# Kernel tuning notes

Measured on AMD Instinct MI355X. Metric: run time of the kernel, lower is better.

The kernel has to match this reference:

```python
import jax, jax.numpy as jnp
import numpy as np

NUM_LAYERS = 2
HIDDEN = 512
INPUT = 512


def _lstm_cell(x, h, c, Wih, Whh, bih, bbh):
    # PyTorch LSTMCell: gates ordered i, f, g, o
    g = x @ Wih.T + bih + h @ Whh.T + bbh  # [B, 4H]
    i, f, gg, o = jnp.split(g, 4, axis=-1)
    c_new = jax.nn.sigmoid(f) * c + jax.nn.sigmoid(i) * jnp.tanh(gg)
    h_new = jax.nn.sigmoid(o) * jnp.tanh(c_new)
    return h_new, c_new


def setup_inputs() -> dict:
    key = jax.random.key(0)
    ks = jax.random.split(key, 8)
    B, T = 64, 512
    s = 1.0 / np.sqrt(HIDDEN)
    return {
        "x": jax.random.normal(ks[0], (B, T, INPUT), dtype=jnp.float32),
        "h0": jax.random.normal(ks[1], (NUM_LAYERS, B, HIDDEN), dtype=jnp.float32),
        "c0": jax.random.normal(ks[2], (NUM_LAYERS, B, HIDDEN), dtype=jnp.float32),
        # stacked per-layer weights (input_size == hidden_size so shapes match)
        "W_ih": jax.random.uniform(ks[3], (NUM_LAYERS, 4 * HIDDEN, INPUT), jnp.float32, -s, s),
        "W_hh": jax.random.uniform(ks[4], (NUM_LAYERS, 4 * HIDDEN, HIDDEN), jnp.float32, -s, s),
        "b_ih": jax.random.uniform(ks[5], (NUM_LAYERS, 4 * HIDDEN), jnp.float32, -s, s),
        "b_hh": jax.random.uniform(ks[6], (NUM_LAYERS, 4 * HIDDEN), jnp.float32, -s, s),
    }


def reference(x, h0, c0, W_ih, W_hh, b_ih, b_hh):
    # x: [B, T, D]; h0/c0: [L, B, H]
    xs = jnp.swapaxes(x, 0, 1)  # [T, B, D] for scan over time

    def step(carry, x_t):
        h, c = carry  # each [L, B, H]
        h_list, c_list = [], []
        inp = x_t
        for j in range(NUM_LAYERS):  # small static unroll over layers
            h_j, c_j = _lstm_cell(inp, h[j], c[j], W_ih[j], W_hh[j], b_ih[j], b_hh[j])
            h_list.append(h_j)
            c_list.append(c_j)
            inp = h_j
        h_new = jnp.stack(h_list, axis=0)
        c_new = jnp.stack(c_list, axis=0)
        return (h_new, c_new), inp  # output of top layer

    (h_fin, c_fin), outs = jax.lax.scan(step, (h0, c0), xs)
    out = jnp.swapaxes(outs, 0, 1)  # [B, T, H]
    return out, h_fin, c_fin
```

## Files before the change

kernel.cpp:

```cpp
#include <hip/hip_runtime.h>
#include <hip/hip_bf16.h>


#define TT 512

using short8 = __attribute__((ext_vector_type(8))) short;
using f32x4  = __attribute__((ext_vector_type(4))) float;

__device__ __forceinline__ short f2bf(float f) {
  unsigned u = __float_as_uint(f);
  u = (u + 0x7fffu + ((u >> 16) & 1u)) >> 16;
  return (short)u;
}
__device__ __forceinline__ float bf2f(short s) {
  return __uint_as_float(((unsigned)(unsigned short)s) << 16);
}
__device__ __forceinline__ float sigf(float x) { return 1.f / (1.f + __expf(-x)); }
__device__ __forceinline__ float tanh_(float x) { return 1.f - 2.f / (__expf(2.f * x) + 1.f); }

__device__ __forceinline__ void ld8_nw(short8* d,
    const short* p0, const short* p1, const short* p2, const short* p3,
    const short* p4, const short* p5, const short* p6, const short* p7) {
  asm volatile(
      "global_load_dwordx4 %0, %8, off sc0 sc1\n\t"
      "global_load_dwordx4 %1, %9, off sc0 sc1\n\t"
      "global_load_dwordx4 %2, %10, off sc0 sc1\n\t"
      "global_load_dwordx4 %3, %11, off sc0 sc1\n\t"
      "global_load_dwordx4 %4, %12, off sc0 sc1\n\t"
      "global_load_dwordx4 %5, %13, off sc0 sc1\n\t"
      "global_load_dwordx4 %6, %14, off sc0 sc1\n\t"
      "global_load_dwordx4 %7, %15, off sc0 sc1"
      : "=&v"(d[0]), "=&v"(d[1]), "=&v"(d[2]), "=&v"(d[3]),
        "=&v"(d[4]), "=&v"(d[5]), "=&v"(d[6]), "=&v"(d[7])
      : "v"(p0), "v"(p1), "v"(p2), "v"(p3),
        "v"(p4), "v"(p5), "v"(p6), "v"(p7)
      : "memory");
}

#define TIE8(A, CNT)                                                        \
  asm volatile(CNT : "+v"(A[0]), "+v"(A[1]), "+v"(A[2]), "+v"(A[3]),        \
                     "+v"(A[4]), "+v"(A[5]), "+v"(A[6]), "+v"(A[7])         \
               ::"memory")

__device__ __forceinline__ void stc_short(short* p, short v) {
  asm volatile("global_store_short %0, %1, off sc0 sc1"
               :: "v"(p), "v"((int)v) : "memory");
}

__global__ __launch_bounds__(256) void conv_x(const float* __restrict__ x,
                                              short* __restrict__ xo) {
  size_t g = (size_t)blockIdx.x * 256 + threadIdx.x;
  size_t i = g * 8;
  float4 v0 = *(const float4*)(x + i);
  float4 v1 = *(const float4*)(x + i + 4);
  short8 r;
  r[0] = f2bf(v0.x); r[1] = f2bf(v0.y); r[2] = f2bf(v0.z); r[3] = f2bf(v0.w);
  r[4] = f2bf(v1.x); r[5] = f2bf(v1.y); r[6] = f2bf(v1.z); r[7] = f2bf(v1.w);
  *(short8*)(xo + (i >> 9) * 1024 + (i & 511)) = r;
}

__global__ __launch_bounds__(256) void conv_w(const float* __restrict__ Wih,
                                              const float* __restrict__ Whh,
                                              short* __restrict__ wp) {
  int g = blockIdx.x * 256 + threadIdx.x;
  int l = g / 393216;
  int rem = g % 393216;
  int j8 = rem / 6144;
  int q8 = rem % 6144;
  int s, hl, bt, c, lane;
  if (q8 < 2048) {
    s = 0; hl = 0;
    int seg = q8 >> 6; bt = seg >> 4; c = seg & 15; lane = q8 & 63;
  } else {
    int q = q8 - 2048;
    s = 1;
    int seg = q >> 6; bt = seg >> 5; c = (seg >> 1) & 15; hl = seg & 1;
    lane = q & 63;
  }
  int r = lane & 15;
  int gg = r >> 2, jj = r & 3;
  int R = gg * 512 + j8 * 8 + bt * 4 + jj;
  int k = c * 32 + (lane >> 4) * 8;
  const float* src = (s ? Whh : Wih) + ((size_t)(l * 2048 + R)) * 512 + k;
  short8 o;
#pragma unroll
  for (int e = 0; e < 8; ++e) {
    float v = src[e];
    short hi = f2bf(v);
    o[e] = hl ? f2bf(v - bf2f(hi)) : hi;
  }
  *(short8*)(wp + (size_t)g * 8) = o;
}

__global__ __launch_bounds__(256) void init_state(const float* __restrict__ h0,
                                                  short* __restrict__ hhi,
                                                  short* __restrict__ hlo,
                                                  unsigned* __restrict__ bar) {
  int i = blockIdx.x * 256 + threadIdx.x;
  int l = i >> 15, bj = i & 32767;
  int b = bj >> 9, j = bj & 511;
  float h = h0[i];
  short hi = f2bf(h);
  int o = (l * 2) * 32768 + (j >> 3) * 512 + b * 8 + (j & 7);
  hhi[o] = hi;
  hlo[o] = f2bf(h - bf2f(hi));
  if (blockIdx.x < 4) bar[blockIdx.x * 256 + threadIdx.x] = 0u;
}

__device__ __forceinline__ void garrive(unsigned* bar, int tid, int slot) {
  __syncthreads();
  if (tid == 0)
    __hip_atomic_fetch_add(&bar[slot * 32], 1u, __ATOMIC_RELAXED,
                           __HIP_MEMORY_SCOPE_AGENT);
}
__device__ __forceinline__ void gwait(unsigned* bar, unsigned target, int tid) {
  if (tid == 0) {
    for (;;) {
      unsigned sum = 0;
#pragma unroll
      for (int r = 0; r < 32; ++r)
        sum += __hip_atomic_load(&bar[r * 32], __ATOMIC_RELAXED,
                                 __HIP_MEMORY_SCOPE_AGENT);
      if (sum >= target) break;
      __builtin_amdgcn_s_sleep(1);
    }
  }
  __syncthreads();
}

__global__ __launch_bounds__(512, 1) void lstm_persist(
    const short* __restrict__ wp, const float* __restrict__ c0,
    const float* __restrict__ bih, const float* __restrict__ bhh,
    short* __restrict__ hhi, short* __restrict__ hlo,
    unsigned* __restrict__ bar, float* __restrict__ out) {
  extern __shared__ char smem[];
  short* lw = (short*)smem;
  float* sG = (float*)(smem + 98304);

  const int tid = threadIdx.x;
  const int layer = blockIdx.x >> 6;
  const int j8 = blockIdx.x & 63;
  const int bslot = blockIdx.x & 31;
  const int wv = tid >> 6;
  const int kq = wv & 3;
  const int ah = wv >> 2;
  const int lane = tid & 63;
  const int m = lane & 15;
  const int koq = lane >> 4;
  const int cbase = kq << 2;

  {
    const short* src = wp + (size_t)(layer * 64 + j8) * 49152;
    for (int i = tid; i < 6144; i += 512)
      *(short8*)(lw + i * 8) = *(const short8*)(src + i * 8);
  }

  const int sb = tid >> 3, sj = tid & 7;
  const int j = (j8 << 3) + sj;
  float creg = c0[layer * 32768 + sb * 512 + j];
  float hf = 0.f;
  float bsum[4];
#pragma unroll
  for (int g = 0; g < 4; ++g)
    bsum[g] = bih[layer * 2048 + g * 512 + j] + bhh[layer * 2048 + g * 512 + j];
  __syncthreads();

  const int br0 = ((ah * 2 + 0) << 4) + m;
  const int br1 = ((ah * 2 + 1) << 4) + m;
  const short* xo = (const short*)out;

  f32x4 acc[2][2];

  auto ih_l0 = [&](int txt) {
#pragma unroll
    for (int cc = 0; cc < 4; ++cc) {
      const int c = cbase + cc;
      const int k = c * 32 + (koq << 3);
      short8 b0 = *(const short8*)(lw + c * 512 + lane * 8);
      short8 b1 = *(const short8*)(lw + (16 + c) * 512 + lane * 8);
#pragma unroll
      for (int it = 0; it < 2; ++it) {
        const int br = it ? br1 : br0;
        short8 a = *(const short8*)(xo + ((size_t)br * TT + txt) * 1024 + k);
        acc[0][it] = __builtin_amdgcn_mfma_f32_16x16x32_bf16(a, b0, acc[0][it], 0, 0, 0);
        acc[1][it] = __builtin_amdgcn_mfma_f32_16x16x32_bf16(a, b1, acc[1][it], 0, 0, 0);
      }
    }
  };

  if (layer == 0) {
#pragma unroll
    for (int u = 0; u < 2; ++u)
#pragma unroll
      for (int v = 0; v < 2; ++v) acc[u][v] = f32x4{0.f, 0.f, 0.f, 0.f};
    ih_l0(0);
  }

#define PA(rX, cc, br) \
  ((rX) + ((((cbase + (cc)) << 2) + koq) << 9) + (br) * 8)

  for (int t = 0; t <= TT; ++t) {
    const int tl = layer ? (t - 1) : t;
    if (tl >= 0 && tl < TT) {
      const int pin = tl & 1, pout = pin ^ 1;
      if (t > 0) gwait(bar, 128u * (unsigned)t, tid);

      short8 Ah[8], Al[8];
      const short* rh = hhi + (layer * 2 + pin) * 32768;
      const short* rl = hlo + (layer * 2 + pin) * 32768;

      if (layer == 0) {
        ld8_nw(Ah, PA(rh, 0, br0), PA(rh, 0, br1), PA(rh, 1, br0), PA(rh, 1, br1),
                   PA(rh, 2, br0), PA(rh, 2, br1), PA(rh, 3, br0), PA(rh, 3, br1));
        ld8_nw(Al, PA(rl, 0, br0), PA(rl, 0, br1), PA(rl, 1, br0), PA(rl, 1, br1),
                   PA(rl, 2, br0), PA(rl, 2, br1), PA(rl, 3, br0), PA(rl, 3, br1));
        TIE8(Ah, "s_waitcnt vmcnt(0)");
        TIE8(Al, "");
      } else {
#pragma unroll
        for (int u = 0; u < 2; ++u)
#pragma unroll
          for (int v = 0; v < 2; ++v) acc[u][v] = f32x4{0.f, 0.f, 0.f, 0.f};
        short8 Ax[8];
        const short* ph = hhi + (t & 1) * 32768;
        ld8_nw(Ax, PA(ph, 0, br0), PA(ph, 0, br1), PA(ph, 1, br0), PA(ph, 1, br1),
                   PA(ph, 2, br0), PA(ph, 2, br1), PA(ph, 3, br0), PA(ph, 3, br1));
        ld8_nw(Ah, PA(rh, 0, br0), PA(rh, 0, br1), PA(rh, 1, br0), PA(rh, 1, br1),
                   PA(rh, 2, br0), PA(rh, 2, br1), PA(rh, 3, br0), PA(rh, 3, br1));
        ld8_nw(Al, PA(rl, 0, br0), PA(rl, 0, br1), PA(rl, 1, br0), PA(rl, 1, br1),
                   PA(rl, 2, br0), PA(rl, 2, br1), PA(rl, 3, br0), PA(rl, 3, br1));
        TIE8(Ax, "s_waitcnt vmcnt(16)");
#pragma unroll
        for (int cc = 0; cc < 4; ++cc) {
          const int c = cbase + cc;
          short8 b0 = *(const short8*)(lw + c * 512 + lane * 8);
          short8 b1 = *(const short8*)(lw + (16 + c) * 512 + lane * 8);
#pragma unroll
          for (int it = 0; it < 2; ++it) {
            short8 a = Ax[cc * 2 + it];
            acc[0][it] = __builtin_amdgcn_mfma_f32_16x16x32_bf16(a, b0, acc[0][it], 0, 0, 0);
            acc[1][it] = __builtin_amdgcn_mfma_f32_16x16x32_bf16(a, b1, acc[1][it], 0, 0, 0);
          }
        }
        TIE8(Ah, "s_waitcnt vmcnt(0)");
        TIE8(Al, "");
      }

#pragma unroll
      for (int cc = 0; cc < 4; ++cc) {
        const int c = cbase + cc;
        short8 bh0 = *(const short8*)(lw + 16384 + (c * 2 + 0) * 512 + lane * 8);
        short8 bl0 = *(const short8*)(lw + 16384 + (c * 2 + 1) * 512 + lane * 8);
        short8 bh1 = *(const short8*)(lw + 16384 + ((16 + c) * 2 + 0) * 512 + lane * 8);
        short8 bl1 = *(const short8*)(lw + 16384 + ((16 + c) * 2 + 1) * 512 + lane * 8);
#pragma unroll
        for (int it = 0; it < 2; ++it) {
          short8 a = Ah[cc * 2 + it];
          short8 al = Al[cc * 2 + it];
          acc[0][it] = __builtin_amdgcn_mfma_f32_16x16x32_bf16(a, bh0, acc[0][it], 0, 0, 0);
          acc[0][it] = __builtin_amdgcn_mfma_f32_16x16x32_bf16(a, bl0, acc[0][it], 0, 0, 0);
          acc[0][it] = __builtin_amdgcn_mfma_f32_16x16x32_bf16(al, bh0, acc[0][it], 0, 0, 0);
          acc[1][it] = __builtin_amdgcn_mfma_f32_16x16x32_bf16(a, bh1, acc[1][it], 0, 0, 0);
          acc[1][it] = __builtin_amdgcn_mfma_f32_16x16x32_bf16(a, bl1, acc[1][it], 0, 0, 0);
          acc[1][it] = __builtin_amdgcn_mfma_f32_16x16x32_bf16(al, bh1, acc[1][it], 0, 0, 0);
        }
      }

#pragma unroll
      for (int bt = 0; bt < 2; ++bt)
#pragma unroll
        for (int it = 0; it < 2; ++it) {
          const int srow = bt * 16 + m;
          const int col = ((ah * 2 + it) << 4) + (koq << 2);
#pragma unroll
          for (int r = 0; r < 4; ++r)
            sG[(kq * 32 + srow) * 66 + col + r] = acc[bt][it][r];
        }
      __syncthreads();

      {
        const int bt = sj >> 2, jl = sj & 3;
        float gv[4];
#pragma unroll
        for (int g = 0; g < 4; ++g) {
          const int s = bt * 16 + g * 4 + jl;
          gv[g] = sG[(0 * 32 + s) * 66 + sb] + sG[(1 * 32 + s) * 66 + sb] +
                  sG[(2 * 32 + s) * 66 + sb] + sG[(3 * 32 + s) * 66 + sb] +
                  bsum[g];
        }
        const float cn = sigf(gv[1]) * creg + sigf(gv[0]) * tanh_(gv[2]);
        const float hn = sigf(gv[3]) * tanh_(cn);
        creg = cn;
        hf = hn;
        const int ho = (layer * 2 + pout) * 32768 + (j8 << 9) + tid;
        const short hb = f2bf(hn);
        stc_short(hhi + ho, hb);
        stc_short(hlo + ho, f2bf(hn - bf2f(hb)));
        if (layer)
          __builtin_nontemporal_store(hn, &out[((size_t)sb * 512 + tl) * 512 + j]);
      }
    }
    if (t < TT) {
      garrive(bar, tid, bslot);
      if (layer == 0 && t + 1 < TT) {
#pragma unroll
        for (int u = 0; u < 2; ++u)
#pragma unroll
          for (int v = 0; v < 2; ++v) acc[u][v] = f32x4{0.f, 0.f, 0.f, 0.f};
        ih_l0(t + 1);
      }
    }
  }

  out[16777216 + layer * 32768 + sb * 512 + j] = hf;
  out[16777216 + 65536 + layer * 32768 + sb * 512 + j] = creg;
}


extern "C" void kernel_launch(void* const* d_in, const int* in_sizes, int n_in,
                              void* d_out, int out_size, void* d_ws,
                              size_t ws_size, hipStream_t stream) {
  const float* x = (const float*)d_in[0];
  const float* h0 = (const float*)d_in[1];
  const float* c0 = (const float*)d_in[2];
  const float* Wih = (const float*)d_in[3];
  const float* Whh = (const float*)d_in[4];
  const float* bih = (const float*)d_in[5];
  const float* bhh = (const float*)d_in[6];
  float* out = (float*)d_out;

  char* ws = (char*)d_ws;
  short* wp = (short*)(ws + 0);
  short* hhi = (short*)(ws + 12582912);
  short* hlo = (short*)(ws + 12845056);
  unsigned* bar = (unsigned*)(ws + 13107200);

  hipFuncSetAttribute(reinterpret_cast<const void*>(lstm_persist),
                      hipFuncAttributeMaxDynamicSharedMemorySize, 132096);

  conv_x<<<8192, 256, 0, stream>>>(x, (short*)out);
  conv_w<<<3072, 256, 0, stream>>>(Wih, Whh, wp);
  init_state<<<256, 256, 0, stream>>>(h0, hhi, hlo, bar);

  void* args[] = {(void*)&wp,  (void*)&c0,  (void*)&bih, (void*)&bhh,
                  (void*)&hhi, (void*)&hlo, (void*)&bar, (void*)&out};
  hipLaunchCooperativeKernel(reinterpret_cast<void*>(lstm_persist), dim3(128),
                             dim3(512), args, 132096, stream);
}
```

Baseline: 2.735 ms.

## Replace global grid barrier with per-block progress flags and layer-decoupled pipelining

Replaces the per-timestep global atomic barrier over all 128 blocks with per-block progress flags that dependent blocks poll. Layer 0 keeps a 4-deep ring of h buffers, so it can run up to three steps ahead of layer 1. Layer 1 waits only on layer 0's step and on its own peers. This is meant to remove global barrier latency and the lockstep coupling between layers. In exchange it adds more polling traffic (64 lanes loading flags) and relies on plain stores plus cache-bypass flags for memory ordering.

```diff
diff --git a/kernel.cpp b/kernel.cpp
--- a/kernel.cpp
+++ b/kernel.cpp
@@ -46,6 +46,29 @@
   asm volatile("global_store_short %0, %1, off sc0 sc1"
                :: "v"(p), "v"((int)v) : "memory");
 }
+__device__ __forceinline__ void stc_int(int* p, int v) {
+  asm volatile("global_store_dword %0, %1, off sc0 sc1"
+               :: "v"(p), "v"(v) : "memory");
+}
+
+__device__ __forceinline__ void pollwait(const int* f0p, const int* f1p,
+                                         int t0, int t1, int tid) {
+  if (tid < 64) {
+    int f0, f1;
+    for (;;) {
+      asm volatile(
+          "global_load_dword %0, %2, off sc0 sc1\n\t"
+          "global_load_dword %1, %3, off sc0 sc1\n\t"
+          "s_waitcnt vmcnt(0)"
+          : "=&v"(f0), "=&v"(f1)
+          : "v"(f0p), "v"(f1p)
+          : "memory");
+      if (__all(f0 >= t0 && f1 >= t1)) break;
+      __builtin_amdgcn_s_sleep(1);
+    }
+  }
+  __syncthreads();
+}
 
 __global__ __launch_bounds__(256) void conv_x(const float* __restrict__ x,
                                               short* __restrict__ xo) {
@@ -93,46 +116,33 @@
 }
 
 __global__ __launch_bounds__(256) void init_state(const float* __restrict__ h0,
-                                                  short* __restrict__ hhi,
-                                                  short* __restrict__ hlo,
-                                                  unsigned* __restrict__ bar) {
+                                                  short* __restrict__ h0hi,
+                                                  short* __restrict__ h0lo,
+                                                  short* __restrict__ h1hi,
+                                                  short* __restrict__ h1lo,
+                                                  int* __restrict__ flags) {
   int i = blockIdx.x * 256 + threadIdx.x;
   int l = i >> 15, bj = i & 32767;
   int b = bj >> 9, j = bj & 511;
   float h = h0[i];
   short hi = f2bf(h);
-  int o = (l * 2) * 32768 + (j >> 3) * 512 + b * 8 + (j & 7);
-  hhi[o] = hi;
-  hlo[o] = f2bf(h - bf2f(hi));
-  if (blockIdx.x < 4) bar[blockIdx.x * 256 + threadIdx.x] = 0u;
-}
-
-__device__ __forceinline__ void garrive(unsigned* bar, int tid, int slot) {
-  __syncthreads();
-  if (tid == 0)
-    __hip_atomic_fetch_add(&bar[slot * 32], 1u, __ATOMIC_RELAXED,
-                           __HIP_MEMORY_SCOPE_AGENT);
-}
-__device__ __forceinline__ void gwait(unsigned* bar, unsigned target, int tid) {
-  if (tid == 0) {
-    for (;;) {
-      unsigned sum = 0;
-#pragma unroll
-      for (int r = 0; r < 32; ++r)
-        sum += __hip_atomic_load(&bar[r * 32], __ATOMIC_RELAXED,
-                                 __HIP_MEMORY_SCOPE_AGENT);
-      if (sum >= target) break;
-      __builtin_amdgcn_s_sleep(1);
-    }
-  }
-  __syncthreads();
+  int o = (j >> 3) * 512 + b * 8 + (j & 7);
+  if (l == 0) {
+    h0hi[3 * 32768 + o] = hi;
+    h0lo[3 * 32768 + o] = f2bf(h - bf2f(hi));
+  } else {
+    h1hi[1 * 32768 + o] = hi;
+    h1lo[1 * 32768 + o] = f2bf(h - bf2f(hi));
+  }
+  if (blockIdx.x == 0 && threadIdx.x < 128) flags[threadIdx.x] = 0;
 }
 
 __global__ __launch_bounds__(512, 1) void lstm_persist(
     const short* __restrict__ wp, const float* __restrict__ c0,
     const float* __restrict__ bih, const float* __restrict__ bhh,
-    short* __restrict__ hhi, short* __restrict__ hlo,
-    unsigned* __restrict__ bar, float* __restrict__ out) {
+    short* __restrict__ h0hi, short* __restrict__ h0lo,
+    short* __restrict__ h1hi, short* __restrict__ h1lo,
+    int* __restrict__ flags, float* __restrict__ out) {
   extern __shared__ char smem[];
   short* lw = (short*)smem;
   float* sG = (float*)(smem + 98304);
@@ -140,7 +150,6 @@
   const int tid = threadIdx.x;
   const int layer = blockIdx.x >> 6;
   const int j8 = blockIdx.x & 63;
-  const int bslot = blockIdx.x & 31;
   const int wv = tid >> 6;
   const int kq = wv & 3;
   const int ah = wv >> 2;
@@ -168,10 +177,65 @@
   const int br0 = ((ah * 2 + 0) << 4) + m;
   const int br1 = ((ah * 2 + 1) << 4) + m;
   const short* xo = (const short*)out;
+  const int* f0p = flags + lane;
+  const int* f1p = flags + 64 + lane;
 
   f32x4 acc[2][2];
 
-  auto ih_l0 = [&](int txt) {
+#define ZACC()                                                   \
+  {                                                              \
+    _Pragma("unroll") for (int u = 0; u < 2; ++u)                \
+        _Pragma("unroll") for (int v = 0; v < 2; ++v)            \
+            acc[u][v] = f32x4{0.f, 0.f, 0.f, 0.f};               \
+  }
+
+#define PA(rX, cc, br) \
+  ((rX) + ((((cbase + (cc)) << 2) + koq) << 9) + (br) * 8)
+
+#define HH_MFMA(Ah, Al)                                                        \
+  _Pragma("unroll") for (int cc = 0; cc < 4; ++cc) {                           \
+    const int c = cbase + cc;                                                  \
+    short8 bh0 = *(const short8*)(lw + 16384 + (c * 2 + 0) * 512 + lane * 8);  \
+    short8 bl0 = *(const short8*)(lw + 16384 + (c * 2 + 1) * 512 + lane * 8);  \
+    short8 bh1 = *(const short8*)(lw + 16384 + ((16 + c) * 2 + 0) * 512 + lane * 8); \
+    short8 bl1 = *(const short8*)(lw + 16384 + ((16 + c) * 2 + 1) * 512 + lane * 8); \
+    _Pragma("unroll") for (int it = 0; it < 2; ++it) {                         \
+      short8 a = Ah[cc * 2 + it];                                              \
+      short8 al = Al[cc * 2 + it];                                             \
+      acc[0][it] = __builtin_amdgcn_mfma_f32_16x16x32_bf16(a, bh0, acc[0][it], 0, 0, 0); \
+      acc[0][it] = __builtin_amdgcn_mfma_f32_16x16x32_bf16(a, bl0, acc[0][it], 0, 0, 0); \
+      acc[0][it] = __builtin_amdgcn_mfma_f32_16x16x32_bf16(al, bh0, acc[0][it], 0, 0, 0); \
+      acc[1][it] = __builtin_amdgcn_mfma_f32_16x16x32_bf16(a, bh1, acc[1][it], 0, 0, 0); \
+      acc[1][it] = __builtin_amdgcn_mfma_f32_16x16x32_bf16(a, bl1, acc[1][it], 0, 0, 0); \
+      acc[1][it] = __builtin_amdgcn_mfma_f32_16x16x32_bf16(al, bh1, acc[1][it], 0, 0, 0); \
+    }                                                                          \
+  }
+
+#define EPILOGUE(CN, HN)                                                       \
+  _Pragma("unroll") for (int bt = 0; bt < 2; ++bt)                             \
+      _Pragma("unroll") for (int it = 0; it < 2; ++it) {                       \
+    const int srow = bt * 16 + m;                                              \
+    const int col = ((ah * 2 + it) << 4) + (koq << 2);                         \
+    _Pragma("unroll") for (int r = 0; r < 4; ++r)                              \
+        sG[(kq * 32 + srow) * 66 + col + r] = acc[bt][it][r];                  \
+  }                                                                            \
+  __syncthreads();                                                             \
+  float CN, HN;                                                                \
+  {                                                                            \
+    const int bt = sj >> 2, jl = sj & 3;                                       \
+    float gv[4];                                                               \
+    _Pragma("unroll") for (int g = 0; g < 4; ++g) {                            \
+      const int s = bt * 16 + g * 4 + jl;                                      \
+      gv[g] = sG[(0 * 32 + s) * 66 + sb] + sG[(1 * 32 + s) * 66 + sb] +        \
+              sG[(2 * 32 + s) * 66 + sb] + sG[(3 * 32 + s) * 66 + sb] +        \
+              bsum[g];                                                         \
+    }                                                                          \
+    CN = sigf(gv[1]) * creg + sigf(gv[0]) * tanh_(gv[2]);                      \
+    HN = sigf(gv[3]) * tanh_(CN);                                              \
+  }
+
+  if (layer == 0) {
+    ZACC();
 #pragma unroll
     for (int cc = 0; cc < 4; ++cc) {
       const int c = cbase + cc;
@@ -181,134 +245,103 @@
 #pragma unroll
       for (int it = 0; it < 2; ++it) {
         const int br = it ? br1 : br0;
-        short8 a = *(const short8*)(xo + ((size_t)br * TT + txt) * 1024 + k);
+        short8 a = *(const short8*)(xo + ((size_t)br * TT + 0) * 1024 + k);
         acc[0][it] = __builtin_amdgcn_mfma_f32_16x16x32_bf16(a, b0, acc[0][it], 0, 0, 0);
         acc[1][it] = __builtin_amdgcn_mfma_f32_16x16x32_bf16(a, b1, acc[1][it], 0, 0, 0);
       }
     }
-  };
-
-  if (layer == 0) {
-#pragma unroll
-    for (int u = 0; u < 2; ++u)
-#pragma unroll
-      for (int v = 0; v < 2; ++v) acc[u][v] = f32x4{0.f, 0.f, 0.f, 0.f};
-    ih_l0(0);
-  }
-
-#define PA(rX, cc, br) \
-  ((rX) + ((((cbase + (cc)) << 2) + koq) << 9) + (br) * 8)
-
-  for (int t = 0; t <= TT; ++t) {
-    const int tl = layer ? (t - 1) : t;
-    if (tl >= 0 && tl < TT) {
-      const int pin = tl & 1, pout = pin ^ 1;
-      if (t > 0) gwait(bar, 128u * (unsigned)t, tid);
+
+    for (int p = 0; p < TT; ++p) {
+      pollwait(f0p, f1p, p, p - 3, tid);
 
       short8 Ah[8], Al[8];
-      const short* rh = hhi + (layer * 2 + pin) * 32768;
-      const short* rl = hlo + (layer * 2 + pin) * 32768;
-
-      if (layer == 0) {
-        ld8_nw(Ah, PA(rh, 0, br0), PA(rh, 0, br1), PA(rh, 1, br0), PA(rh, 1, br1),
-                   PA(rh, 2, br0), PA(rh, 2, br1), PA(rh, 3, br0), PA(rh, 3, br1));
-        ld8_nw(Al, PA(rl, 0, br0), PA(rl, 0, br1), PA(rl, 1, br0), PA(rl, 1, br1),
-                   PA(rl, 2, br0), PA(rl, 2, br1), PA(rl, 3, br0), PA(rl, 3, br1));
-        TIE8(Ah, "s_waitcnt vmcnt(0)");
-        TIE8(Al, "");
-      } else {
-#pragma unroll
-        for (int u = 0; u < 2; ++u)
-#pragma unroll
-          for (int v = 0; v < 2; ++v) acc[u][v] = f32x4{0.f, 0.f, 0.f, 0.f};
-        short8 Ax[8];
-        const short* ph = hhi + (t & 1) * 32768;
-        ld8_nw(Ax, PA(ph, 0, br0), PA(ph, 0, br1), PA(ph, 1, br0), PA(ph, 1, br1),
-                   PA(ph, 2, br0), PA(ph, 2, br1), PA(ph, 3, br0), PA(ph, 3, br1));
-        ld8_nw(Ah, PA(rh, 0, br0), PA(rh, 0, br1), PA(rh, 1, br0), PA(rh, 1, br1),
-                   PA(rh, 2, br0), PA(rh, 2, br1), PA(rh, 3, br0), PA(rh, 3, br1));
-        ld8_nw(Al, PA(rl, 0, br0), PA(rl, 0, br1), PA(rl, 1, br0), PA(rl, 1, br1),
-                   PA(rl, 2, br0), PA(rl, 2, br1), PA(rl, 3, br0), PA(rl, 3, br1));
-        TIE8(Ax, "s_waitcnt vmcnt(16)");
+      const short* rh = h0hi + ((p - 1) & 3) * 32768;
+      const short* rl = h0lo + ((p - 1) & 3) * 32768;
+      ld8_nw(Ah, PA(rh, 0, br0), PA(rh, 0, br1), PA(rh, 1, br0), PA(rh, 1, br1),
+                 PA(rh, 2, br0), PA(rh, 2, br1), PA(rh, 3, br0), PA(rh, 3, br1));
+      ld8_nw(Al, PA(rl, 0, br0), PA(rl, 0, br1), PA(rl, 1, br0), PA(rl, 1, br1),
+                 PA(rl, 2, br0), PA(rl, 2, br1), PA(rl, 3, br0), PA(rl, 3, br1));
+      TIE8(Ah, "s_waitcnt vmcnt(0)");
+      TIE8(Al, "");
+      HH_MFMA(Ah, Al);
+
+      EPILOGUE(cn, hn);
+      creg = cn;
+      hf = hn;
+      {
+        short* dh = h0hi + (p & 3) * 32768 + (j8 << 9) + tid;
+        short* dl = h0lo + (p & 3) * 32768 + (j8 << 9) + tid;
+        const short hb = f2bf(hn);
+        stc_short(dh, hb);
+        stc_short(dl, f2bf(hn - bf2f(hb)));
+      }
+      __syncthreads();
+      if (tid == 0) stc_int(flags + j8, p + 1);
+
+      if (p + 1 < TT) {
+        ZACC();
 #pragma unroll
         for (int cc = 0; cc < 4; ++cc) {
           const int c = cbase + cc;
+          const int k = c * 32 + (koq << 3);
           short8 b0 = *(const short8*)(lw + c * 512 + lane * 8);
           short8 b1 = *(const short8*)(lw + (16 + c) * 512 + lane * 8);
 #pragma unroll
           for (int it = 0; it < 2; ++it) {
-            short8 a = Ax[cc * 2 + it];
+            const int br = it ? br1 : br0;
+            short8 a = *(const short8*)(xo + ((size_t)br * TT + p + 1) * 1024 + k);
             acc[0][it] = __builtin_amdgcn_mfma_f32_16x16x32_bf16(a, b0, acc[0][it], 0, 0, 0);
             acc[1][it] = __builtin_amdgcn_mfma_f32_16x16x32_bf16(a, b1, acc[1][it], 0, 0, 0);
           }
         }
-        TIE8(Ah, "s_waitcnt vmcnt(0)");
-        TIE8(Al, "");
-      }
-
+      }
+    }
+  } else {
+    for (int tau = 1; tau <= TT; ++tau) {
+      const int tl = tau - 1;
+      pollwait(f0p, f1p, tau, tau - 1, tid);
+
+      ZACC();
+      short8 Ax[8], Ah[8], Al[8];
+      const short* ph = h0hi + (tl & 3) * 32768;
+      const short* rh = h1hi + (tau & 1) * 32768;
+      const short* rl = h1lo + (tau & 1) * 32768;
+      ld8_nw(Ax, PA(ph, 0, br0), PA(ph, 0, br1), PA(ph, 1, br0), PA(ph, 1, br1),
+                 PA(ph, 2, br0), PA(ph, 2, br1), PA(ph, 3, br0), PA(ph, 3, br1));
+      ld8_nw(Ah, PA(rh, 0, br0), PA(rh, 0, br1), PA(rh, 1, br0), PA(rh, 1, br1),
+                 PA(rh, 2, br0), PA(rh, 2, br1), PA(rh, 3, br0), PA(rh, 3, br1));
+      ld8_nw(Al, PA(rl, 0, br0), PA(rl, 0, br1), PA(rl, 1, br0), PA(rl, 1, br1),
+                 PA(rl, 2, br0), PA(rl, 2, br1), PA(rl, 3, br0), PA(rl, 3, br1));
+      TIE8(Ax, "s_waitcnt vmcnt(16)");
 #pragma unroll
       for (int cc = 0; cc < 4; ++cc) {
         const int c = cbase + cc;
-        short8 bh0 = *(const short8*)(lw + 16384 + (c * 2 + 0) * 512 + lane * 8);
-        short8 bl0 = *(const short8*)(lw + 16384 + (c * 2 + 1) * 512 + lane * 8);
-        short8 bh1 = *(const short8*)(lw + 16384 + ((16 + c) * 2 + 0) * 512 + lane * 8);
-        short8 bl1 = *(const short8*)(lw + 16384 + ((16 + c) * 2 + 1) * 512 + lane * 8);
+        short8 b0 = *(const short8*)(lw + c * 512 + lane * 8);
+        short8 b1 = *(const short8*)(lw + (16 + c) * 512 + lane * 8);
 #pragma unroll
         for (int it = 0; it < 2; ++it) {
-          short8 a = Ah[cc * 2 + it];
-          short8 al = Al[cc * 2 + it];
-          acc[0][it] = __builtin_amdgcn_mfma_f32_16x16x32_bf16(a, bh0, acc[0][it], 0, 0, 0);
-          acc[0][it] = __builtin_amdgcn_mfma_f32_16x16x32_bf16(a, bl0, acc[0][it], 0, 0, 0);
-          acc[0][it] = __builtin_amdgcn_mfma_f32_16x16x32_bf16(al, bh0, acc[0][it], 0, 0, 0);
-          acc[1][it] = __builtin_amdgcn_mfma_f32_16x16x32_bf16(a, bh1, acc[1][it], 0, 0, 0);
-          acc[1][it] = __builtin_amdgcn_mfma_f32_16x16x32_bf16(a, bl1, acc[1][it], 0, 0, 0);
-          acc[1][it] = __builtin_amdgcn_mfma_f32_16x16x32_bf16(al, bh1, acc[1][it], 0, 0, 0);
+          short8 a = Ax[cc * 2 + it];
+          acc[0][it] = __builtin_amdgcn_mfma_f32_16x16x32_bf16(a, b0, acc[0][it], 0, 0, 0);
+          acc[1][it] = __builtin_amdgcn_mfma_f32_16x16x32_bf16(a, b1, acc[1][it], 0, 0, 0);
         }
       }
-
-#pragma unroll
-      for (int bt = 0; bt < 2; ++bt)
-#pragma unroll
-        for (int it = 0; it < 2; ++it) {
-          const int srow = bt * 16 + m;
-          const int col = ((ah * 2 + it) << 4) + (koq << 2);
-#pragma unroll
-          for (int r = 0; r < 4; ++r)
-            sG[(kq * 32 + srow) * 66 + col + r] = acc[bt][it][r];
-        }
+      TIE8(Ah, "s_waitcnt vmcnt(0)");
+      TIE8(Al, "");
+      HH_MFMA(Ah, Al);
+
+      EPILOGUE(cn, hn);
+      creg = cn;
+      hf = hn;
+      {
+        short* dh = h1hi + ((tau + 1) & 1) * 32768 + (j8 << 9) + tid;
+        short* dl = h1lo + ((tau + 1) & 1) * 32768 + (j8 << 9) + tid;
+        const short hb = f2bf(hn);
+        stc_short(dh, hb);
+        stc_short(dl, f2bf(hn - bf2f(hb)));
+      }
       __syncthreads();
-
-      {
-        const int bt = sj >> 2, jl = sj & 3;
-        float gv[4];
-#pragma unroll
-        for (int g = 0; g < 4; ++g) {
-          const int s = bt * 16 + g * 4 + jl;
-          gv[g] = sG[(0 * 32 + s) * 66 + sb] + sG[(1 * 32 + s) * 66 + sb] +
-                  sG[(2 * 32 + s) * 66 + sb] + sG[(3 * 32 + s) * 66 + sb] +
-                  bsum[g];
-        }
-        const float cn = sigf(gv[1]) * creg + sigf(gv[0]) * tanh_(gv[2]);
-        const float hn = sigf(gv[3]) * tanh_(cn);
-        creg = cn;
-        hf = hn;
-        const int ho = (layer * 2 + pout) * 32768 + (j8 << 9) + tid;
-        const short hb = f2bf(hn);
-        stc_short(hhi + ho, hb);
-        stc_short(hlo + ho, f2bf(hn - bf2f(hb)));
-        if (layer)
-          __builtin_nontemporal_store(hn, &out[((size_t)sb * 512 + tl) * 512 + j]);
-      }
-    }
-    if (t < TT) {
-      garrive(bar, tid, bslot);
-      if (layer == 0 && t + 1 < TT) {
-#pragma unroll
-        for (int u = 0; u < 2; ++u)
-#pragma unroll
-          for (int v = 0; v < 2; ++v) acc[u][v] = f32x4{0.f, 0.f, 0.f, 0.f};
-        ih_l0(t + 1);
-      }
+      if (tid == 0) stc_int(flags + 64 + j8, tau);
+      __builtin_nontemporal_store(hn, &out[((size_t)sb * 512 + tl) * 512 + j]);
     }
   }
 
@@ -330,20 +363,23 @@
   float* out = (float*)d_out;
 
   char* ws = (char*)d_ws;
-  short* wp = (short*)(ws + 0);
-  short* hhi = (short*)(ws + 12582912);
-  short* hlo = (short*)(ws + 12845056);
-  unsigned* bar = (unsigned*)(ws + 13107200);
+  short* wp   = (short*)(ws + 0);
+  short* h0hi = (short*)(ws + 12582912);
+  short* h0lo = (short*)(ws + 12845056);
+  short* h1hi = (short*)(ws + 13107200);
+  short* h1lo = (short*)(ws + 13238272);
+  int*  flags = (int*)(ws + 13369344);
 
   hipFuncSetAttribute(reinterpret_cast<const void*>(lstm_persist),
                       hipFuncAttributeMaxDynamicSharedMemorySize, 132096);
 
   conv_x<<<8192, 256, 0, stream>>>(x, (short*)out);
   conv_w<<<3072, 256, 0, stream>>>(Wih, Whh, wp);
-  init_state<<<256, 256, 0, stream>>>(h0, hhi, hlo, bar);
-
-  void* args[] = {(void*)&wp,  (void*)&c0,  (void*)&bih, (void*)&bhh,
-                  (void*)&hhi, (void*)&hlo, (void*)&bar, (void*)&out};
+  init_state<<<256, 256, 0, stream>>>(h0, h0hi, h0lo, h1hi, h1lo, flags);
+
+  void* args[] = {(void*)&wp,   (void*)&c0,   (void*)&bih,  (void*)&bhh,
+                  (void*)&h0hi, (void*)&h0lo, (void*)&h1hi, (void*)&h1lo,
+                  (void*)&flags, (void*)&out};
   hipLaunchCooperativeKernel(reinterpret_cast<void*>(lstm_persist), dim3(128),
                              dim3(512), args, 132096, stream);
 }
```

After: 3.071 ms. +12.3%, slower.
